# Kernel tuning notes

Hardware: AMD Instinct MI355X
Metric: run time of the kernel (lower is better)

## Reference

```python
import jax, jax.numpy as jnp
import numpy as np


def gcn_conv(x, edge_index, W, b):
    # PyG GCNConv with normalize=True: add self-loops, symmetric D^-1/2 A D^-1/2,
    # transform then aggregate messages source->target, then add bias.
    N = x.shape[0]
    row, col = edge_index[0], edge_index[1]  # row: source, col: target
    loop = jnp.arange(N, dtype=edge_index.dtype)
    row = jnp.concatenate([row, loop])
    col = jnp.concatenate([col, loop])
    ones = jnp.ones(row.shape[0], dtype=x.dtype)
    deg = jax.ops.segment_sum(ones, col, num_segments=N)
    dinv = jnp.where(deg > 0, jax.lax.rsqrt(deg), 0.0)
    norm = dinv[row] * dinv[col]            # [E+N]
    h = x @ W                                # [N, d_out] transform first (cheaper aggregation)
    msgs = h[row] * norm[:, None]            # gather + scale
    out = jax.ops.segment_sum(msgs, col, num_segments=N)  # scatter-add to targets
    return out + b


def setup_inputs() -> dict:
    key = jax.random.key(0)
    k = jax.random.split(key, 6)
    N, D, H, C, E = 100000, 256, 32, 2, 3200000
    x = jax.random.normal(k[0], (N, D), dtype=jnp.float32)
    edge_index = jax.random.randint(k[1], (2, E), 0, N, dtype=jnp.int64)
    # glorot-style init for GCN weights
    W1 = jax.random.normal(k[2], (D, H), dtype=jnp.float32) * np.sqrt(2.0 / (D + H))
    b1 = jnp.zeros((H,), dtype=jnp.float32)
    W2 = jax.random.normal(k[3], (H, C), dtype=jnp.float32) * np.sqrt(2.0 / (H + C))
    b2 = jnp.zeros((C,), dtype=jnp.float32)
    return {"x": x, "edge_index": edge_index, "W1": W1, "b1": b1, "W2": W2, "b2": b2}


def reference(x, edge_index, W1, b1, W2, b2):
    # CRD: GCNConv -> relu -> dropout(p=0.5, eval mode -> identity)
    h = jax.nn.relu(gcn_conv(x, edge_index, W1, b1))
    # CLS: GCNConv -> log_softmax over classes
    logits = gcn_conv(h, edge_index, W2, b2)
    return jax.nn.log_softmax(logits, axis=1)
```

## Files before the change

kernel.cpp:

```cpp
#include <hip/hip_runtime.h>
#include <hip/hip_fp16.h>
#include <math.h>

#define DIV_UP(a,b) (((a)+(b)-1)/(b))

typedef _Float16 f16x8 __attribute__((ext_vector_type(8)));
typedef float    f32x4 __attribute__((ext_vector_type(4)));

#define SHIFT 9
#define TPB   (1 << SHIFT)
#define LMASK (TPB - 1)
#define CHUNK 4096

__global__ __launch_bounds__(256) void k_init(int* __restrict__ gcur, int cap,
                                              int* __restrict__ offsets,
                                              const float* __restrict__ W,
                                              _Float16* __restrict__ Wl, int N, int E) {
    const int t = threadIdx.x;
    gcur[t] = t * cap;
    if (t == 0) offsets[N] = E;
#pragma unroll
    for (int c = 0; c < 4; ++c) {
        int chunk = t + 256 * c;
        int m0 = chunk & 15;
        int q  = (chunk >> 4) & 3;
        int ct = (chunk >> 6) & 1;
        int kc = chunk >> 7;
        int n  = ct * 16 + m0;
        f16x8 v;
#pragma unroll
        for (int j = 0; j < 8; ++j)
            v[j] = (_Float16)W[(kc * 32 + q * 8 + j) * 32 + n];
        *(f16x8*)&Wl[(size_t)chunk * 8] = v;
    }
}

__global__ __launch_bounds__(256) void k_fat(const float* __restrict__ x,
                                             const _Float16* __restrict__ Wl,
                                             __half* __restrict__ h1,
                                             const int* __restrict__ row,
                                             const int* __restrict__ col,
                                             int* __restrict__ gcur,
                                             unsigned* __restrict__ binned,
                                             int E, int N, int nchunk) {
    __shared__ __align__(16) char smem[24608];
    const int t = threadIdx.x;
    const int bid = blockIdx.x;
    const bool isBin = (bid < 2 * nchunk) && (bid & 1);

    if (!isBin) {
        const int gb = (bid < 2 * nchunk) ? (bid >> 1) : (bid - nchunk);
        _Float16* WlT = (_Float16*)smem;

        const uint4* Wg4 = (const uint4*)Wl;
#pragma unroll
        for (int i = 0; i < 4; ++i)
            ((uint4*)WlT)[t + 256 * i] = Wg4[t + 256 * i];
        __syncthreads();

        const int lane = t & 63;
        const int wv   = t >> 6;
        const int m    = lane & 15;
        const int q    = lane >> 4;

        const int rowA   = gb * 64 + wv * 16 + m;
        const int rclamp = min(rowA, N - 1);
        const float* xr  = x + (long long)rclamp * 256 + q * 8;

        float4 va[16];
#pragma unroll
        for (int kc = 0; kc < 8; ++kc) {
            va[2 * kc]     = *(const float4*)(xr + kc * 32);
            va[2 * kc + 1] = *(const float4*)(xr + kc * 32 + 4);
        }
        __builtin_amdgcn_sched_barrier(0);

        f32x4 c0 = {0.f, 0.f, 0.f, 0.f}, c1 = {0.f, 0.f, 0.f, 0.f};
#pragma unroll
        for (int kc = 0; kc < 8; ++kc) {
            f16x8 b0 = *(const f16x8*)&WlT[(size_t)((kc * 2 + 0) * 64 + lane) * 8];
            f16x8 b1 = *(const f16x8*)&WlT[(size_t)((kc * 2 + 1) * 64 + lane) * 8];
            float4 v0 = va[2 * kc], v1 = va[2 * kc + 1];
            f16x8 a;
            a[0] = (_Float16)v0.x; a[1] = (_Float16)v0.y;
            a[2] = (_Float16)v0.z; a[3] = (_Float16)v0.w;
            a[4] = (_Float16)v1.x; a[5] = (_Float16)v1.y;
            a[6] = (_Float16)v1.z; a[7] = (_Float16)v1.w;
            c0 = __builtin_amdgcn_mfma_f32_16x16x32_f16(a, b0, c0, 0, 0, 0);
            c1 = __builtin_amdgcn_mfma_f32_16x16x32_f16(a, b1, c1, 0, 0, 0);
        }

        const int orow = gb * 64 + wv * 16 + q * 4;
#pragma unroll
        for (int r = 0; r < 4; ++r) {
            int gr = orow + r;
            if (gr < N) {
                h1[gr * 32 + m]      = __float2half(c0[r]);
                h1[gr * 32 + 16 + m] = __float2half(c1[r]);
            }
        }
    } else {
        int* hist  = (int*)smem;
        int* loff  = hist + 256;
        int* gbase = loff + 256;
        int* lcur  = gbase + 256;
        unsigned* staged     = (unsigned*)(smem + 4096);
        unsigned char* binOf = (unsigned char*)(smem + 4096 + 16384);
        int* wtot            = (int*)(smem + 4096 + 16384 + 4096);

        const int base = (bid >> 1) * CHUNK;
        const int n = min(CHUNK, E - base);

        hist[t] = 0;
        __syncthreads();

        unsigned pk[CHUNK / 256];
        int bn[CHUNK / 256];
#pragma unroll
        for (int k = 0; k < CHUNK / 256; ++k) {
            int i = base + t + k * 256;
            if (i < E) {
                int c = col[i], r = row[i];
                bn[k] = c >> SHIFT;
                pk[k] = ((unsigned)r << SHIFT) | (unsigned)(c & LMASK);
                atomicAdd(&hist[bn[k]], 1);
            } else bn[k] = -1;
        }
        __syncthreads();

        const int hv = hist[t];
        int sc = hv;
#pragma unroll
        for (int s = 1; s < 64; s <<= 1) {
            int y = __shfl_up(sc, s, 64);
            if ((t & 63) >= s) sc += y;
        }
        if ((t & 63) == 63) wtot[t >> 6] = sc;
        __syncthreads();
        int woff = 0;
#pragma unroll
        for (int j = 0; j < 3; ++j) if (j < (t >> 6)) woff += wtot[j];
        const int excl = sc + woff - hv;
        gbase[t] = hv ? atomicAdd(&gcur[t], hv) : 0;
        lcur[t] = excl;
        loff[t] = excl;
        __syncthreads();

#pragma unroll
        for (int k = 0; k < CHUNK / 256; ++k) {
            if (bn[k] >= 0) {
                int p = atomicAdd(&lcur[bn[k]], 1);
                staged[p] = pk[k];
                binOf[p] = (unsigned char)bn[k];
            }
        }
        __syncthreads();

        for (int i = t; i < n; i += 256) {
            int bb = binOf[i];
            binned[gbase[bb] + (i - loff[bb])] = staged[i];
        }
    }
}

__global__ __launch_bounds__(1024) void k_csr2(const unsigned* __restrict__ binned,
                                               const int* __restrict__ gcur, int cap,
                                               int* __restrict__ offsets,
                                               float* __restrict__ dinv,
                                               int* __restrict__ srcs,
                                               __half* __restrict__ h1, int N) {
    __shared__ int h[TPB];
    __shared__ int cur[TPB];
    __shared__ float sdi[TPB];
    __shared__ int wred[16];
    const int t = threadIdx.x, b = blockIdx.x;
    const int lane = t & 63, wv = t >> 6;
    const int beg = b * cap, end = gcur[b];

    int contrib = (t < 256 && t < b) ? (gcur[t] - t * cap) : 0;
#pragma unroll
    for (int s = 1; s < 64; s <<= 1) contrib += __shfl_xor(contrib, s, 64);
    if (t < TPB) h[t] = 0;
    if (lane == 0 && wv < 4) wred[wv] = contrib;
    __syncthreads();
    const int obase = wred[0] + wred[1] + wred[2] + wred[3];

    for (int i = beg + t; i < end; i += 1024)
        atomicAdd(&h[binned[i] & LMASK], 1);
    __syncthreads();

    const int cnt = (t < TPB) ? h[t] : 0;
    int sc = cnt;
#pragma unroll
    for (int s = 1; s < 64; s <<= 1) {
        int y = __shfl_up(sc, s, 64);
        if (lane >= s) sc += y;
    }
    if (t < TPB && lane == 63) wred[8 + wv] = sc;
    __syncthreads();
    if (t < TPB) {
        int woff = 0;
        for (int j = 0; j < wv; ++j) woff += wred[8 + j];
        const int excl = sc + woff - cnt;
        const int g = (b << SHIFT) + t;
        const int pos0 = obase + excl;
        float di = 0.f;
        if (g < N) {
            offsets[g] = pos0;
            di = rsqrtf((float)(1 + cnt));
            dinv[g] = di;
        }
        cur[t] = pos0;
        sdi[t] = di;
    }
    __syncthreads();

    for (int i = beg + t; i < end; i += 1024) {
        unsigned v = binned[i];
        int pos = atomicAdd(&cur[v & LMASK], 1);
        srcs[pos] = (int)(v >> SHIFT);
    }

    const int node = (b << SHIFT) + (t >> 1);
    if (node < N) {
        float di = sdi[t >> 1];
        uint4* hp4 = (uint4*)(h1 + (size_t)node * 32) + (t & 1) * 2;
#pragma unroll
        for (int k4 = 0; k4 < 2; ++k4) {
            uint4 v = hp4[k4];
            __half2* ph = (__half2*)&v;
#pragma unroll
            for (int k2 = 0; k2 < 4; ++k2) {
                float2 u = __half22float2(ph[k2]);
                ph[k2] = __floats2half2_rn(u.x * di, u.y * di);
            }
            hp4[k4] = v;
        }
    }
}

__global__ void k_agg1(const int* __restrict__ offsets, const int* __restrict__ srcs,
                       const float* __restrict__ dinv, const __half* __restrict__ h1w,
                       const float* __restrict__ b1, const float* __restrict__ W2,
                       __half2* __restrict__ tw, int N) {
    long long g = (long long)blockIdx.x * blockDim.x + threadIdx.x;
    int node = (int)(g >> 5), f = (int)(g & 31);
    if (node >= N) return;
    const int sub = f >> 2, q = f & 3;
    const int beg = offsets[node], end = offsets[node + 1];
    const uint4* h4 = (const uint4*)h1w;

    float a0 = 0.f, a1 = 0.f, a2 = 0.f, a3 = 0.f;
    float a4 = 0.f, a5 = 0.f, a6 = 0.f, a7 = 0.f;

    for (int j = beg; j < end; j += 16) {
        int e0 = j + sub, e1 = j + 8 + sub;
        int s0 = srcs[min(e0, end - 1)];
        int s1 = srcs[min(e1, end - 1)];
        float m0 = (e0 < end) ? 1.f : 0.f;
        float m1 = (e1 < end) ? 1.f : 0.f;
        uint4 rv0 = h4[s0 * 4 + q];
        uint4 rv1 = h4[s1 * 4 + q];
        __half2 p; float2 u;
        p = *(__half2*)&rv0.x; u = __half22float2(p); a0 = fmaf(u.x, m0, a0); a1 = fmaf(u.y, m0, a1);
        p = *(__half2*)&rv0.y; u = __half22float2(p); a2 = fmaf(u.x, m0, a2); a3 = fmaf(u.y, m0, a3);
        p = *(__half2*)&rv0.z; u = __half22float2(p); a4 = fmaf(u.x, m0, a4); a5 = fmaf(u.y, m0, a5);
        p = *(__half2*)&rv0.w; u = __half22float2(p); a6 = fmaf(u.x, m0, a6); a7 = fmaf(u.y, m0, a7);
        p = *(__half2*)&rv1.x; u = __half22float2(p); a0 = fmaf(u.x, m1, a0); a1 = fmaf(u.y, m1, a1);
        p = *(__half2*)&rv1.y; u = __half22float2(p); a2 = fmaf(u.x, m1, a2); a3 = fmaf(u.y, m1, a3);
        p = *(__half2*)&rv1.z; u = __half22float2(p); a4 = fmaf(u.x, m1, a4); a5 = fmaf(u.y, m1, a5);
        p = *(__half2*)&rv1.w; u = __half22float2(p); a6 = fmaf(u.x, m1, a6); a7 = fmaf(u.y, m1, a7);
    }
#pragma unroll
    for (int s = 4; s < 32; s <<= 1) {
        a0 += __shfl_xor(a0, s, 32); a1 += __shfl_xor(a1, s, 32);
        a2 += __shfl_xor(a2, s, 32); a3 += __shfl_xor(a3, s, 32);
        a4 += __shfl_xor(a4, s, 32); a5 += __shfl_xor(a5, s, 32);
        a6 += __shfl_xor(a6, s, 32); a7 += __shfl_xor(a7, s, 32);
    }
    if (sub == 0) {
        float di = dinv[node];
        uint4 rv = h4[node * 4 + q];
        float sf[8];
        {
            __half2 p; float2 u;
            p = *(__half2*)&rv.x; u = __half22float2(p); sf[0] = u.x; sf[1] = u.y;
            p = *(__half2*)&rv.y; u = __half22float2(p); sf[2] = u.x; sf[3] = u.y;
            p = *(__half2*)&rv.z; u = __half22float2(p); sf[4] = u.x; sf[5] = u.y;
            p = *(__half2*)&rv.w; u = __half22float2(p); sf[6] = u.x; sf[7] = u.y;
        }
        float av[8] = {a0, a1, a2, a3, a4, a5, a6, a7};
        float t0 = 0.f, t1 = 0.f;
#pragma unroll
        for (int k = 0; k < 8; ++k) {
            int feat = q * 8 + k;
            float hv = fmaf(di, av[k] + sf[k], b1[feat]);
            hv = fmaxf(hv, 0.f);
            t0 = fmaf(hv, W2[feat * 2 + 0], t0);
            t1 = fmaf(hv, W2[feat * 2 + 1], t1);
        }
        t0 += __shfl_xor(t0, 1, 32); t0 += __shfl_xor(t0, 2, 32);
        t1 += __shfl_xor(t1, 1, 32); t1 += __shfl_xor(t1, 2, 32);
        if (q == 0) tw[node] = __floats2half2_rn(di * t0, di * t1);
    }
}

__global__ void k_agg2(const int* __restrict__ offsets, const int* __restrict__ srcs,
                       const float* __restrict__ dinv, const __half2* __restrict__ tw,
                       const float* __restrict__ b2, float* __restrict__ out, int N) {
    long long g = (long long)blockIdx.x * blockDim.x + threadIdx.x;
    int node = (int)(g >> 4), f = (int)(g & 15);
    if (node >= N) return;
    int beg = offsets[node], end = offsets[node + 1];
    float a0 = 0.f, a1 = 0.f;
    for (int j = beg + f; j < end; j += 16) {
        int s = srcs[j];
        float2 u = __half22float2(tw[s]);
        a0 += u.x;
        a1 += u.y;
    }
#pragma unroll
    for (int s = 8; s; s >>= 1) {
        a0 += __shfl_xor(a0, s, 64);
        a1 += __shfl_xor(a1, s, 64);
    }
    if (f == 0) {
        float di = dinv[node];
        float2 u = __half22float2(tw[node]);
        float z0 = di * (a0 + u.x) + b2[0];
        float z1 = di * (a1 + u.y) + b2[1];
        float m = fmaxf(z0, z1);
        float lse = m + logf(expf(z0 - m) + expf(z1 - m));
        ((float2*)out)[node] = float2{z0 - lse, z1 - lse};
    }
}

extern "C" void kernel_launch(void* const* d_in, const int* in_sizes, int n_in,
                              void* d_out, int out_size, void* d_ws, size_t ws_size,
                              hipStream_t stream) {
    const float* x  = (const float*)d_in[0];
    const int*   ei = (const int*)d_in[1];
    const float* W1 = (const float*)d_in[2];
    const float* b1 = (const float*)d_in[3];
    const float* W2 = (const float*)d_in[4];
    const float* b2 = (const float*)d_in[5];

    const int H = in_sizes[3];
    const int D = in_sizes[2] / H;
    const int N = in_sizes[0] / D;
    const int E = in_sizes[1] / 2;
    (void)H; (void)n_in; (void)out_size; (void)ws_size;

    const int* row = ei;
    const int* col = ei + E;

    const int K_used = ((N - 1) >> SHIFT) + 1;
    const int cap    = (DIV_UP(E, K_used) * 5 / 4 + 255) & ~255;
    const int nchunk = DIV_UP(E, CHUNK);
    const int gemmB  = DIV_UP(N, 64);

    char* p = (char*)d_ws;
    auto alloc = [&](size_t bytes) { char* q = p; p += (bytes + 255) & ~(size_t)255; return q; };
    int*      offsets = (int*)     alloc((size_t)(N + 1) * 4);
    int*      gcur    = (int*)     alloc(256 * 4);
    _Float16* Wl      = (_Float16*)alloc(8192 * 2);
    float*    dinv    = (float*)   alloc((size_t)N * 4);
    unsigned* binned  = (unsigned*)alloc((size_t)K_used * cap * 4);
    __half*   h1      = (__half*)  alloc((size_t)N * 32 * 2);
    int*      srcs    = (int*)     alloc((size_t)E * 4);
    __half2*  tw      = (__half2*) alloc((size_t)N * 4);

    k_init <<<1, 256, 0, stream>>>(gcur, cap, offsets, W1, Wl, N, E);
    k_fat  <<<gemmB + nchunk, 256, 0, stream>>>(x, Wl, h1, row, col, gcur, binned, E, N, nchunk);
    k_csr2 <<<K_used, 1024, 0, stream>>>(binned, gcur, cap, offsets, dinv, srcs, h1, N);
    k_agg1 <<<(int)DIV_UP((long long)N * 32, 256), 256, 0, stream>>>(offsets, srcs, dinv, h1, b1, W2, tw, N);
    k_agg2 <<<(int)DIV_UP((long long)N * 16, 256), 256, 0, stream>>>(offsets, srcs, dinv, tw, b2, (float*)d_out, N);
}
```

Baseline: 274.5 us.

## Split fused GEMM/binning kernel and move dinv source scaling into aggregation

The fused kernel that interleaved GEMM blocks with edge-binning blocks is split into two separate launches, k_bin and k_gemm, each with its own statically sized shared memory. The pass in k_csr2 that pre-scaled h1 rows by dinv is removed. k_agg1 now gathers dinv[src] per edge and applies it at aggregation time, and scales the self term explicitly. This drops a read-modify-write pass over h1 and the shared dinv buffer, but adds a dinv gather per edge and loses the overlap between the GEMM and binning work. An asm barrier is also added to keep the x loads issued ahead of the MFMA loop.

Result: slower. 298.5 us (+8.8%).

```diff
diff --git a/kernel.cpp b/kernel.cpp
--- a/kernel.cpp
+++ b/kernel.cpp
@@ -35,130 +35,131 @@
     }
 }
 
-__global__ __launch_bounds__(256) void k_fat(const float* __restrict__ x,
-                                             const _Float16* __restrict__ Wl,
-                                             __half* __restrict__ h1,
-                                             const int* __restrict__ row,
+__global__ __launch_bounds__(256) void k_bin(const int* __restrict__ row,
                                              const int* __restrict__ col,
                                              int* __restrict__ gcur,
                                              unsigned* __restrict__ binned,
-                                             int E, int N, int nchunk) {
-    __shared__ __align__(16) char smem[24608];
+                                             int E) {
+    __shared__ int hist[256];
+    __shared__ int loff[256];
+    __shared__ int gbase[256];
+    __shared__ int lcur[256];
+    __shared__ unsigned staged[CHUNK];
+    __shared__ unsigned char binOf[CHUNK];
+    __shared__ int wtot[4];
+
     const int t = threadIdx.x;
-    const int bid = blockIdx.x;
-    const bool isBin = (bid < 2 * nchunk) && (bid & 1);
-
-    if (!isBin) {
-        const int gb = (bid < 2 * nchunk) ? (bid >> 1) : (bid - nchunk);
-        _Float16* WlT = (_Float16*)smem;
-
-        const uint4* Wg4 = (const uint4*)Wl;
-#pragma unroll
-        for (int i = 0; i < 4; ++i)
-            ((uint4*)WlT)[t + 256 * i] = Wg4[t + 256 * i];
-        __syncthreads();
-
-        const int lane = t & 63;
-        const int wv   = t >> 6;
-        const int m    = lane & 15;
-        const int q    = lane >> 4;
-
-        const int rowA   = gb * 64 + wv * 16 + m;
-        const int rclamp = min(rowA, N - 1);
-        const float* xr  = x + (long long)rclamp * 256 + q * 8;
-
-        float4 va[16];
-#pragma unroll
-        for (int kc = 0; kc < 8; ++kc) {
-            va[2 * kc]     = *(const float4*)(xr + kc * 32);
-            va[2 * kc + 1] = *(const float4*)(xr + kc * 32 + 4);
-        }
-        __builtin_amdgcn_sched_barrier(0);
-
-        f32x4 c0 = {0.f, 0.f, 0.f, 0.f}, c1 = {0.f, 0.f, 0.f, 0.f};
-#pragma unroll
-        for (int kc = 0; kc < 8; ++kc) {
-            f16x8 b0 = *(const f16x8*)&WlT[(size_t)((kc * 2 + 0) * 64 + lane) * 8];
-            f16x8 b1 = *(const f16x8*)&WlT[(size_t)((kc * 2 + 1) * 64 + lane) * 8];
-            float4 v0 = va[2 * kc], v1 = va[2 * kc + 1];
-            f16x8 a;
-            a[0] = (_Float16)v0.x; a[1] = (_Float16)v0.y;
-            a[2] = (_Float16)v0.z; a[3] = (_Float16)v0.w;
-            a[4] = (_Float16)v1.x; a[5] = (_Float16)v1.y;
-            a[6] = (_Float16)v1.z; a[7] = (_Float16)v1.w;
-            c0 = __builtin_amdgcn_mfma_f32_16x16x32_f16(a, b0, c0, 0, 0, 0);
-            c1 = __builtin_amdgcn_mfma_f32_16x16x32_f16(a, b1, c1, 0, 0, 0);
-        }
-
-        const int orow = gb * 64 + wv * 16 + q * 4;
-#pragma unroll
-        for (int r = 0; r < 4; ++r) {
-            int gr = orow + r;
-            if (gr < N) {
-                h1[gr * 32 + m]      = __float2half(c0[r]);
-                h1[gr * 32 + 16 + m] = __float2half(c1[r]);
-            }
-        }
-    } else {
-        int* hist  = (int*)smem;
-        int* loff  = hist + 256;
-        int* gbase = loff + 256;
-        int* lcur  = gbase + 256;
-        unsigned* staged     = (unsigned*)(smem + 4096);
-        unsigned char* binOf = (unsigned char*)(smem + 4096 + 16384);
-        int* wtot            = (int*)(smem + 4096 + 16384 + 4096);
-
-        const int base = (bid >> 1) * CHUNK;
-        const int n = min(CHUNK, E - base);
-
-        hist[t] = 0;
-        __syncthreads();
-
-        unsigned pk[CHUNK / 256];
-        int bn[CHUNK / 256];
-#pragma unroll
-        for (int k = 0; k < CHUNK / 256; ++k) {
-            int i = base + t + k * 256;
-            if (i < E) {
-                int c = col[i], r = row[i];
-                bn[k] = c >> SHIFT;
-                pk[k] = ((unsigned)r << SHIFT) | (unsigned)(c & LMASK);
-                atomicAdd(&hist[bn[k]], 1);
-            } else bn[k] = -1;
-        }
-        __syncthreads();
-
-        const int hv = hist[t];
-        int sc = hv;
-#pragma unroll
-        for (int s = 1; s < 64; s <<= 1) {
-            int y = __shfl_up(sc, s, 64);
-            if ((t & 63) >= s) sc += y;
-        }
-        if ((t & 63) == 63) wtot[t >> 6] = sc;
-        __syncthreads();
-        int woff = 0;
-#pragma unroll
-        for (int j = 0; j < 3; ++j) if (j < (t >> 6)) woff += wtot[j];
-        const int excl = sc + woff - hv;
-        gbase[t] = hv ? atomicAdd(&gcur[t], hv) : 0;
-        lcur[t] = excl;
-        loff[t] = excl;
-        __syncthreads();
-
-#pragma unroll
-        for (int k = 0; k < CHUNK / 256; ++k) {
-            if (bn[k] >= 0) {
-                int p = atomicAdd(&lcur[bn[k]], 1);
-                staged[p] = pk[k];
-                binOf[p] = (unsigned char)bn[k];
-            }
-        }
-        __syncthreads();
-
-        for (int i = t; i < n; i += 256) {
-            int bb = binOf[i];
-            binned[gbase[bb] + (i - loff[bb])] = staged[i];
+    const int base = blockIdx.x * CHUNK;
+    const int n = min(CHUNK, E - base);
+
+    hist[t] = 0;
+    __syncthreads();
+
+    unsigned pk[CHUNK / 256];
+    int bn[CHUNK / 256];
+#pragma unroll
+    for (int k = 0; k < CHUNK / 256; ++k) {
+        int i = base + t + k * 256;
+        if (i < E) {
+            int c = col[i], r = row[i];
+            bn[k] = c >> SHIFT;
+            pk[k] = ((unsigned)r << SHIFT) | (unsigned)(c & LMASK);
+            atomicAdd(&hist[bn[k]], 1);
+        } else bn[k] = -1;
+    }
+    __syncthreads();
+
+    const int hv = hist[t];
+    int sc = hv;
+#pragma unroll
+    for (int s = 1; s < 64; s <<= 1) {
+        int y = __shfl_up(sc, s, 64);
+        if ((t & 63) >= s) sc += y;
+    }
+    if ((t & 63) == 63) wtot[t >> 6] = sc;
+    __syncthreads();
+    int woff = 0;
+#pragma unroll
+    for (int j = 0; j < 3; ++j) if (j < (t >> 6)) woff += wtot[j];
+    const int excl = sc + woff - hv;
+    gbase[t] = hv ? atomicAdd(&gcur[t], hv) : 0;
+    lcur[t] = excl;
+    loff[t] = excl;
+    __syncthreads();
+
+#pragma unroll
+    for (int k = 0; k < CHUNK / 256; ++k) {
+        if (bn[k] >= 0) {
+            int p = atomicAdd(&lcur[bn[k]], 1);
+            staged[p] = pk[k];
+            binOf[p] = (unsigned char)bn[k];
+        }
+    }
+    __syncthreads();
+
+    for (int i = t; i < n; i += 256) {
+        int bb = binOf[i];
+        binned[gbase[bb] + (i - loff[bb])] = staged[i];
+    }
+}
+
+__global__ __launch_bounds__(256) void k_gemm(const float* __restrict__ x,
+                                              const _Float16* __restrict__ Wl,
+                                              __half* __restrict__ h1, int N) {
+    __shared__ __align__(16) _Float16 WlT[8192];
+    const int t = threadIdx.x;
+    const int gb = blockIdx.x;
+
+    const uint4* Wg4 = (const uint4*)Wl;
+#pragma unroll
+    for (int i = 0; i < 4; ++i)
+        ((uint4*)WlT)[t + 256 * i] = Wg4[t + 256 * i];
+    __syncthreads();
+
+    const int lane = t & 63;
+    const int wv   = t >> 6;
+    const int m    = lane & 15;
+    const int q    = lane >> 4;
+
+    const int rowA   = gb * 64 + wv * 16 + m;
+    const int rclamp = min(rowA, N - 1);
+    const float* xr  = x + (long long)rclamp * 256 + q * 8;
+
+    float4 va[16];
+#pragma unroll
+    for (int kc = 0; kc < 8; ++kc) {
+        va[2 * kc]     = *(const float4*)(xr + kc * 32);
+        va[2 * kc + 1] = *(const float4*)(xr + kc * 32 + 4);
+    }
+    asm volatile("" ::
+        "v"(va[0].x),  "v"(va[1].x),  "v"(va[2].x),  "v"(va[3].x),
+        "v"(va[4].x),  "v"(va[5].x),  "v"(va[6].x),  "v"(va[7].x),
+        "v"(va[8].x),  "v"(va[9].x),  "v"(va[10].x), "v"(va[11].x),
+        "v"(va[12].x), "v"(va[13].x), "v"(va[14].x), "v"(va[15].x));
+    __builtin_amdgcn_sched_barrier(0);
+
+    f32x4 c0 = {0.f, 0.f, 0.f, 0.f}, c1 = {0.f, 0.f, 0.f, 0.f};
+#pragma unroll
+    for (int kc = 0; kc < 8; ++kc) {
+        f16x8 b0 = *(const f16x8*)&WlT[(size_t)((kc * 2 + 0) * 64 + lane) * 8];
+        f16x8 b1 = *(const f16x8*)&WlT[(size_t)((kc * 2 + 1) * 64 + lane) * 8];
+        float4 v0 = va[2 * kc], v1 = va[2 * kc + 1];
+        f16x8 a;
+        a[0] = (_Float16)v0.x; a[1] = (_Float16)v0.y;
+        a[2] = (_Float16)v0.z; a[3] = (_Float16)v0.w;
+        a[4] = (_Float16)v1.x; a[5] = (_Float16)v1.y;
+        a[6] = (_Float16)v1.z; a[7] = (_Float16)v1.w;
+        c0 = __builtin_amdgcn_mfma_f32_16x16x32_f16(a, b0, c0, 0, 0, 0);
+        c1 = __builtin_amdgcn_mfma_f32_16x16x32_f16(a, b1, c1, 0, 0, 0);
+    }
+
+    const int orow = gb * 64 + wv * 16 + q * 4;
+#pragma unroll
+    for (int r = 0; r < 4; ++r) {
+        int gr = orow + r;
+        if (gr < N) {
+            h1[gr * 32 + m]      = __float2half(c0[r]);
+            h1[gr * 32 + 16 + m] = __float2half(c1[r]);
         }
     }
 }
@@ -167,11 +168,9 @@
                                                const int* __restrict__ gcur, int cap,
                                                int* __restrict__ offsets,
                                                float* __restrict__ dinv,
-                                               int* __restrict__ srcs,
-                                               __half* __restrict__ h1, int N) {
+                                               int* __restrict__ srcs, int N) {
     __shared__ int h[TPB];
     __shared__ int cur[TPB];
-    __shared__ float sdi[TPB];
     __shared__ int wred[16];
     const int t = threadIdx.x, b = blockIdx.x;
     const int lane = t & 63, wv = t >> 6;
@@ -204,14 +203,11 @@
         const int excl = sc + woff - cnt;
         const int g = (b << SHIFT) + t;
         const int pos0 = obase + excl;
-        float di = 0.f;
         if (g < N) {
             offsets[g] = pos0;
-            di = rsqrtf((float)(1 + cnt));
-            dinv[g] = di;
+            dinv[g] = rsqrtf((float)(1 + cnt));
         }
         cur[t] = pos0;
-        sdi[t] = di;
     }
     __syncthreads();
 
@@ -220,27 +216,10 @@
         int pos = atomicAdd(&cur[v & LMASK], 1);
         srcs[pos] = (int)(v >> SHIFT);
     }
-
-    const int node = (b << SHIFT) + (t >> 1);
-    if (node < N) {
-        float di = sdi[t >> 1];
-        uint4* hp4 = (uint4*)(h1 + (size_t)node * 32) + (t & 1) * 2;
-#pragma unroll
-        for (int k4 = 0; k4 < 2; ++k4) {
-            uint4 v = hp4[k4];
-            __half2* ph = (__half2*)&v;
-#pragma unroll
-            for (int k2 = 0; k2 < 4; ++k2) {
-                float2 u = __half22float2(ph[k2]);
-                ph[k2] = __floats2half2_rn(u.x * di, u.y * di);
-            }
-            hp4[k4] = v;
-        }
-    }
 }
 
 __global__ void k_agg1(const int* __restrict__ offsets, const int* __restrict__ srcs,
-                       const float* __restrict__ dinv, const __half* __restrict__ h1w,
+                       const float* __restrict__ dinv, const __half* __restrict__ h1,
                        const float* __restrict__ b1, const float* __restrict__ W2,
                        __half2* __restrict__ tw, int N) {
     long long g = (long long)blockIdx.x * blockDim.x + threadIdx.x;
@@ -248,7 +227,7 @@
     if (node >= N) return;
     const int sub = f >> 2, q = f & 3;
     const int beg = offsets[node], end = offsets[node + 1];
-    const uint4* h4 = (const uint4*)h1w;
+    const uint4* h4 = (const uint4*)h1;
 
     float a0 = 0.f, a1 = 0.f, a2 = 0.f, a3 = 0.f;
     float a4 = 0.f, a5 = 0.f, a6 = 0.f, a7 = 0.f;
@@ -257,19 +236,19 @@
         int e0 = j + sub, e1 = j + 8 + sub;
         int s0 = srcs[min(e0, end - 1)];
         int s1 = srcs[min(e1, end - 1)];
-        float m0 = (e0 < end) ? 1.f : 0.f;
-        float m1 = (e1 < end) ? 1.f : 0.f;
+        float dm0 = dinv[s0] * ((e0 < end) ? 1.f : 0.f);
+        float dm1 = dinv[s1] * ((e1 < end) ? 1.f : 0.f);
         uint4 rv0 = h4[s0 * 4 + q];
         uint4 rv1 = h4[s1 * 4 + q];
         __half2 p; float2 u;
-        p = *(__half2*)&rv0.x; u = __half22float2(p); a0 = fmaf(u.x, m0, a0); a1 = fmaf(u.y, m0, a1);
-        p = *(__half2*)&rv0.y; u = __half22float2(p); a2 = fmaf(u.x, m0, a2); a3 = fmaf(u.y, m0, a3);
-        p = *(__half2*)&rv0.z; u = __half22float2(p); a4 = fmaf(u.x, m0, a4); a5 = fmaf(u.y, m0, a5);
-        p = *(__half2*)&rv0.w; u = __half22float2(p); a6 = fmaf(u.x, m0, a6); a7 = fmaf(u.y, m0, a7);
-        p = *(__half2*)&rv1.x; u = __half22float2(p); a0 = fmaf(u.x, m1, a0); a1 = fmaf(u.y, m1, a1);
-        p = *(__half2*)&rv1.y; u = __half22float2(p); a2 = fmaf(u.x, m1, a2); a3 = fmaf(u.y, m1, a3);
-        p = *(__half2*)&rv1.z; u = __half22float2(p); a4 = fmaf(u.x, m1, a4); a5 = fmaf(u.y, m1, a5);
-        p = *(__half2*)&rv1.w; u = __half22float2(p); a6 = fmaf(u.x, m1, a6); a7 = fmaf(u.y, m1, a7);
+        p = *(__half2*)&rv0.x; u = __half22float2(p); a0 = fmaf(u.x, dm0, a0); a1 = fmaf(u.y, dm0, a1);
+        p = *(__half2*)&rv0.y; u = __half22float2(p); a2 = fmaf(u.x, dm0, a2); a3 = fmaf(u.y, dm0, a3);
+        p = *(__half2*)&rv0.z; u = __half22float2(p); a4 = fmaf(u.x, dm0, a4); a5 = fmaf(u.y, dm0, a5);
+        p = *(__half2*)&rv0.w; u = __half22float2(p); a6 = fmaf(u.x, dm0, a6); a7 = fmaf(u.y, dm0, a7);
+        p = *(__half2*)&rv1.x; u = __half22float2(p); a0 = fmaf(u.x, dm1, a0); a1 = fmaf(u.y, dm1, a1);
+        p = *(__half2*)&rv1.y; u = __half22float2(p); a2 = fmaf(u.x, dm1, a2); a3 = fmaf(u.y, dm1, a3);
+        p = *(__half2*)&rv1.z; u = __half22float2(p); a4 = fmaf(u.x, dm1, a4); a5 = fmaf(u.y, dm1, a5);
+        p = *(__half2*)&rv1.w; u = __half22float2(p); a6 = fmaf(u.x, dm1, a6); a7 = fmaf(u.y, dm1, a7);
     }
 #pragma unroll
     for (int s = 4; s < 32; s <<= 1) {
@@ -294,7 +273,7 @@
 #pragma unroll
         for (int k = 0; k < 8; ++k) {
             int feat = q * 8 + k;
-            float hv = fmaf(di, av[k] + sf[k], b1[feat]);
+            float hv = fmaf(di, av[k] + di * sf[k], b1[feat]);
             hv = fmaxf(hv, 0.f);
             t0 = fmaf(hv, W2[feat * 2 + 0], t0);
             t1 = fmaf(hv, W2[feat * 2 + 1], t1);
@@ -371,8 +350,9 @@
     __half2*  tw      = (__half2*) alloc((size_t)N * 4);
 
     k_init <<<1, 256, 0, stream>>>(gcur, cap, offsets, W1, Wl, N, E);
-    k_fat  <<<gemmB + nchunk, 256, 0, stream>>>(x, Wl, h1, row, col, gcur, binned, E, N, nchunk);
-    k_csr2 <<<K_used, 1024, 0, stream>>>(binned, gcur, cap, offsets, dinv, srcs, h1, N);
+    k_bin  <<<nchunk, 256, 0, stream>>>(row, col, gcur, binned, E);
+    k_gemm <<<gemmB, 256, 0, stream>>>(x, Wl, h1, N);
+    k_csr2 <<<K_used, 1024, 0, stream>>>(binned, gcur, cap, offsets, dinv, srcs, N);
     k_agg1 <<<(int)DIV_UP((long long)N * 32, 256), 256, 0, stream>>>(offsets, srcs, dinv, h1, b1, W2, tw, N);
     k_agg2 <<<(int)DIV_UP((long long)N * 16, 256), 256, 0, stream>>>(offsets, srcs, dinv, tw, b2, (float*)d_out, N);
 }
```

## Split CSR build per bin across two blocks handling node halves

Applied to the files above, without the earlier changes.

The CSR construction kernel now launches two 512-thread blocks per destination bin instead of one 1024-thread block. Each block scans the whole bin but only counts and scatters edges whose local node index falls in its half. The second half offsets its positions by a count of the other half's edges. This doubles the block count from about 196 to about 391, giving better CU coverage on a chip with 256 CUs. The cost is that each block reads the full binned array twice, doubling global reads of that buffer.

Result: slower. 280.4 us (+2.2%).

```diff
diff --git a/kernel.cpp b/kernel.cpp
--- a/kernel.cpp
+++ b/kernel.cpp
@@ -163,47 +163,62 @@
     }
 }
 
-__global__ __launch_bounds__(1024) void k_csr2(const unsigned* __restrict__ binned,
-                                               const int* __restrict__ gcur, int cap,
-                                               int* __restrict__ offsets,
-                                               float* __restrict__ dinv,
-                                               int* __restrict__ srcs,
-                                               __half* __restrict__ h1, int N) {
-    __shared__ int h[TPB];
-    __shared__ int cur[TPB];
-    __shared__ float sdi[TPB];
-    __shared__ int wred[16];
-    const int t = threadIdx.x, b = blockIdx.x;
+__global__ __launch_bounds__(512) void k_csr2(const unsigned* __restrict__ binned,
+                                              const int* __restrict__ gcur, int cap,
+                                              int* __restrict__ offsets,
+                                              float* __restrict__ dinv,
+                                              int* __restrict__ srcs,
+                                              __half* __restrict__ h1, int N) {
+    __shared__ int h[256];
+    __shared__ int cur[256];
+    __shared__ float sdi[256];
+    __shared__ int wred[12];
+    const int t = threadIdx.x, bb = blockIdx.x;
+    const int b = bb >> 1, half = bb & 1;
     const int lane = t & 63, wv = t >> 6;
     const int beg = b * cap, end = gcur[b];
 
     int contrib = (t < 256 && t < b) ? (gcur[t] - t * cap) : 0;
 #pragma unroll
     for (int s = 1; s < 64; s <<= 1) contrib += __shfl_xor(contrib, s, 64);
-    if (t < TPB) h[t] = 0;
+    if (t < 256) h[t] = 0;
     if (lane == 0 && wv < 4) wred[wv] = contrib;
     __syncthreads();
     const int obase = wred[0] + wred[1] + wred[2] + wred[3];
 
-    for (int i = beg + t; i < end; i += 1024)
-        atomicAdd(&h[binned[i] & LMASK], 1);
+    int other = 0;
+    for (int i = beg + t; i < end; i += 512) {
+        unsigned v = binned[i];
+        int loc = v & LMASK;
+        if ((loc >> 8) == half) atomicAdd(&h[loc & 255], 1);
+        else ++other;
+    }
+#pragma unroll
+    for (int s = 1; s < 64; s <<= 1) other += __shfl_xor(other, s, 64);
+    if (lane == 0) wred[4 + wv] = other;
     __syncthreads();
 
-    const int cnt = (t < TPB) ? h[t] : 0;
+    const int cnt = (t < 256) ? h[t] : 0;
     int sc = cnt;
 #pragma unroll
     for (int s = 1; s < 64; s <<= 1) {
         int y = __shfl_up(sc, s, 64);
         if (lane >= s) sc += y;
     }
-    if (t < TPB && lane == 63) wred[8 + wv] = sc;
+    if (t < 256 && lane == 63) wred[wv] = sc;
     __syncthreads();
-    if (t < TPB) {
+
+    int base2 = 0;
+    if (half) {
+#pragma unroll
+        for (int j = 0; j < 8; ++j) base2 += wred[4 + j];
+    }
+    if (t < 256) {
         int woff = 0;
-        for (int j = 0; j < wv; ++j) woff += wred[8 + j];
+        for (int j = 0; j < wv; ++j) woff += wred[j];
         const int excl = sc + woff - cnt;
-        const int g = (b << SHIFT) + t;
-        const int pos0 = obase + excl;
+        const int pos0 = obase + base2 + excl;
+        const int g = (b << SHIFT) + (half << 8) + t;
         float di = 0.f;
         if (g < N) {
             offsets[g] = pos0;
@@ -215,13 +230,16 @@
     }
     __syncthreads();
 
-    for (int i = beg + t; i < end; i += 1024) {
+    for (int i = beg + t; i < end; i += 512) {
         unsigned v = binned[i];
-        int pos = atomicAdd(&cur[v & LMASK], 1);
-        srcs[pos] = (int)(v >> SHIFT);
-    }
-
-    const int node = (b << SHIFT) + (t >> 1);
+        int loc = v & LMASK;
+        if ((loc >> 8) == half) {
+            int pos = atomicAdd(&cur[loc & 255], 1);
+            srcs[pos] = (int)(v >> SHIFT);
+        }
+    }
+
+    const int node = (b << SHIFT) + (half << 8) + (t >> 1);
     if (node < N) {
         float di = sdi[t >> 1];
         uint4* hp4 = (uint4*)(h1 + (size_t)node * 32) + (t & 1) * 2;
@@ -372,7 +390,7 @@
 
     k_init <<<1, 256, 0, stream>>>(gcur, cap, offsets, W1, Wl, N, E);
     k_fat  <<<gemmB + nchunk, 256, 0, stream>>>(x, Wl, h1, row, col, gcur, binned, E, N, nchunk);
-    k_csr2 <<<K_used, 1024, 0, stream>>>(binned, gcur, cap, offsets, dinv, srcs, h1, N);
+    k_csr2 <<<2 * K_used, 512, 0, stream>>>(binned, gcur, cap, offsets, dinv, srcs, h1, N);
     k_agg1 <<<(int)DIV_UP((long long)N * 32, 256), 256, 0, stream>>>(offsets, srcs, dinv, h1, b1, W2, tw, N);
     k_agg2 <<<(int)DIV_UP((long long)N * 16, 256), 256, 0, stream>>>(offsets, srcs, dinv, tw, b2, (float*)d_out, N);
 }
```
